# Kernel tuning notes

Measured on AMD Instinct MI355X. Metric: run time of the kernel, lower is better.

Reference implementation:

```python
import jax, jax.numpy as jnp
import numpy as np

KP_EXTENT = 0.05
N_Q = 40000   # query points
N_S = 40000   # support points
K = 32        # neighbors per query
P = 15        # kernel points
IN_DIM = 64
OUT_DIM = 128


def setup_inputs() -> dict:
    key = jax.random.key(0)
    k1, k2, k3, k4, k5, k6 = jax.random.split(key, 6)
    q_pts = jax.random.uniform(k1, (N_Q, 3), dtype=jnp.float32)
    s_pts = jax.random.uniform(k2, (N_S, 3), dtype=jnp.float32)
    # indices in [0, N_S]; value N_S hits the appended shadow row
    neighbor_idxs = jax.random.randint(k3, (N_Q, K), 0, N_S + 1)
    x = jax.random.normal(k4, (N_S, IN_DIM), dtype=jnp.float32)
    weights = jax.random.normal(k5, (P, IN_DIM, OUT_DIM), dtype=jnp.float32) * 0.05
    kernel_points = jax.random.normal(k6, (P, 3), dtype=jnp.float32) * 0.06
    return {"q_pts": q_pts, "s_pts": s_pts, "neighbor_idxs": neighbor_idxs,
            "x": x, "weights": weights, "kernel_points": kernel_points}


def reference(q_pts, s_pts, neighbor_idxs, x, weights, kernel_points):
    # Append shadow support point. NOTE: the original does
    # zeros_like(s_pts[:1,:] + 1e6) which is exactly zeros, so shadow = origin.
    s_pad = jnp.concatenate([s_pts, jnp.zeros_like(s_pts[:1, :])], axis=0)
    # Gather neighbor coordinates, center on queries: [N, K, 3]
    neighbors = s_pad[neighbor_idxs] - q_pts[:, None, :]
    # Distances to every kernel point: [N, K, P]
    diff = neighbors[:, :, None, :] - kernel_points[None, None, :, :]
    sq_distances = jnp.sum(diff * diff, axis=3)
    all_weights = jnp.clip(1.0 - jnp.sqrt(sq_distances) / KP_EXTENT, 0.0)
    all_weights = jnp.transpose(all_weights, (0, 2, 1))  # [N, P, K]
    # Gather neighbor features with zero shadow row: [N, K, D_in]
    feats = jnp.concatenate([x, jnp.zeros_like(x[:1, :])], axis=0)
    neighbors_x = feats[neighbor_idxs]
    # Kernel-point weighted aggregation: [N, P, D_in] -> [P, N, D_in]
    weighted_features = jnp.transpose(jnp.matmul(all_weights, neighbors_x), (1, 0, 2))
    # Per-kernel-point linear map: [P, N, D_out], then sum over kernel points
    kernel_outputs = jnp.matmul(weighted_features, weights)
    output_features = jnp.sum(kernel_outputs, axis=0)  # [N, D_out]
    # Normalize by count of "valid" neighbors (feature-sum > 0 heuristic)
    neighbor_features_sum = jnp.sum(neighbors_x, axis=-1)          # [N, K]
    neighbor_num = jnp.sum(neighbor_features_sum > 0.0, axis=-1)   # [N]
    neighbor_num = jnp.maximum(neighbor_num, 1).astype(output_features.dtype)
    return output_features / neighbor_num[:, None]
```

## Files before the change

kernel.cpp:

```cpp
#include <hip/hip_runtime.h>
#include <hip/hip_bf16.h>

#define N_Q     40000
#define N_S     40000
#define KK      32
#define PP      15
#define IN_DIM  64
#define OUT_DIM 128


__global__ __launch_bounds__(256) void prep_kernel(
    const float* __restrict__ x, const float* __restrict__ s_pts,
    const float* __restrict__ weights,
    float4* __restrict__ packed, __hip_bfloat162* __restrict__ wbf) {
  const int b = blockIdx.x;
  if (b < 2500) {
    const int t = b * 256 + threadIdx.x;
    const int row = t >> 4;
    const int sub = t & 15;
    float4 v = reinterpret_cast<const float4*>(x + (size_t)row * IN_DIM)[sub];
    float s = (v.x + v.y) + (v.z + v.w);
    s += __shfl_xor(s, 1, 64);
    s += __shfl_xor(s, 2, 64);
    s += __shfl_xor(s, 4, 64);
    s += __shfl_xor(s, 8, 64);
    if (sub == 0) {
      float4 pkt;
      pkt.x = s_pts[row * 3 + 0];
      pkt.y = s_pts[row * 3 + 1];
      pkt.z = s_pts[row * 3 + 2];
      pkt.w = (s > 0.0f) ? 1.0f : 0.0f;
      packed[row] = pkt;
    }
    if (t == 1) {
      float4 z; z.x = 0.f; z.y = 0.f; z.z = 0.f; z.w = 0.f;
      packed[N_S] = z;
    }
  } else {
    const int t = (b - 2500) * 256 + threadIdx.x;
    float2 w2 = reinterpret_cast<const float2*>(weights)[t];
    __hip_bfloat162 h;
    h.x = __float2bfloat16(w2.x);
    h.y = __float2bfloat16(w2.y);
    wbf[t] = h;
  }
}

__global__ __launch_bounds__(256) void kpconv_fused_kernel(
    const float* __restrict__ q_pts, const int* __restrict__ nidx,
    const float* __restrict__ x, const float* __restrict__ kpts,
    const float4* __restrict__ packed, const __hip_bfloat162* __restrict__ wbf,
    float* __restrict__ out) {
  const int tid  = blockIdx.x * 256 + threadIdx.x;
  const int lane = threadIdx.x & 63;
  const int n  = tid >> 5;
  const int nA = (tid & ~63) >> 5;

  float kx[PP], ky[PP], kz[PP];
  #pragma unroll
  for (int p = 0; p < PP; ++p) {
    kx[p] = kpts[p * 3 + 0];
    ky[p] = kpts[p * 3 + 1];
    kz[p] = kpts[p * 3 + 2];
  }

  const int id = nidx[tid];
  const float4 sp = packed[id];
  const bool real = (id < N_S);

  const float ox = sp.x - q_pts[n * 3 + 0];
  const float oy = sp.y - q_pts[n * 3 + 1];
  const float oz = sp.z - q_pts[n * 3 + 2];

  unsigned long long bal = __ballot(sp.w != 0.0f);
  unsigned int half = (lane < 32) ? (unsigned int)bal
                                  : (unsigned int)(bal >> 32);
  int num = (int)__popc(half);
  if (num < 1) num = 1;
  const float invnum = 1.0f / (float)num;

  float a0 = 0.f, a1 = 0.f;
  float b0 = 0.f, b1 = 0.f;

  #pragma unroll
  for (int p = 0; p < PP; ++p) {
    const float dx = ox - kx[p];
    const float dy = oy - ky[p];
    const float dz = oz - kz[p];
    const float d2 = dx * dx + dy * dy + dz * dz;
    const bool hit = real && (d2 < 0.0025f);
    unsigned long long b2 = __ballot(hit);
    if (b2 != 0ull) {
      const float wn = hit ? (1.0f - 20.0f * sqrtf(d2)) * invnum : 0.0f;
      while (b2) {
        const int j = __ffsll(b2) - 1;
        b2 &= b2 - 1;
        const float wj  = __shfl(wn, j);
        const int   idj = __shfl(id, j);
        const float* xr = x + (size_t)idj * IN_DIM;
        const __hip_bfloat162* wp =
            wbf + (size_t)p * (IN_DIM * OUT_DIM / 2) + lane;
        float h0 = 0.f, h1 = 0.f;
        #pragma unroll 4
        for (int d4 = 0; d4 < IN_DIM / 4; ++d4) {
          const float4 xv4 =
              *reinterpret_cast<const float4*>(xr + 4 * d4);
          #pragma unroll
          for (int dd = 0; dd < 4; ++dd) {
            const int d = 4 * d4 + dd;
            const __hip_bfloat162 w2 = wp[(size_t)d * (OUT_DIM / 2)];
            const float xd = (dd == 0) ? xv4.x : (dd == 1) ? xv4.y
                           : (dd == 2) ? xv4.z : xv4.w;
            h0 += xd * __bfloat162float(w2.x);
            h1 += xd * __bfloat162float(w2.y);
          }
        }
        if (j < 32) { a0 += wj * h0; a1 += wj * h1; }
        else        { b0 += wj * h0; b1 += wj * h1; }
      }
    }
  }

  float2 ra; ra.x = a0; ra.y = a1;
  float2 rb; rb.x = b0; rb.y = b1;
  *reinterpret_cast<float2*>(out + (size_t)nA * OUT_DIM + 2 * lane) = ra;
  *reinterpret_cast<float2*>(out + (size_t)(nA + 1) * OUT_DIM + 2 * lane) = rb;
}

extern "C" void kernel_launch(void* const* d_in, const int* in_sizes, int n_in,
                              void* d_out, int out_size, void* d_ws, size_t ws_size,
                              hipStream_t stream) {
  const float* q_pts   = (const float*)d_in[0];
  const float* s_pts   = (const float*)d_in[1];
  const int*   nidx    = (const int*)d_in[2];
  const float* x       = (const float*)d_in[3];
  const float* weights = (const float*)d_in[4];
  const float* kpts    = (const float*)d_in[5];
  float* out = (float*)d_out;

  char* ws = (char*)d_ws;
  float4*          packed = (float4*)ws;
  __hip_bfloat162* wbf    = (__hip_bfloat162*)(ws + (1u << 20));

  prep_kernel<<<2740, 256, 0, stream>>>(x, s_pts, weights, packed, wbf);
  kpconv_fused_kernel<<<(N_Q * KK) / 256, 256, 0, stream>>>(
      q_pts, nidx, x, kpts, packed, wbf, out);
}
```

Measured before the change: 105.1 us.

## Use bf16 MFMA for per-hit feature projection and prefilter neighbors by radius

```diff
diff --git a/kernel.cpp b/kernel.cpp
--- a/kernel.cpp
+++ b/kernel.cpp
@@ -1,5 +1,4 @@
 #include <hip/hip_runtime.h>
-#include <hip/hip_bf16.h>
 
 #define N_Q     40000
 #define N_S     40000
@@ -8,11 +7,20 @@
 #define IN_DIM  64
 #define OUT_DIM 128
 
+typedef __attribute__((ext_vector_type(8))) short short8;
+typedef __attribute__((ext_vector_type(4))) float floatx4;
+
+static __device__ __forceinline__ short f2bf(float f) {
+  union { float f; unsigned u; } v; v.f = f;
+  unsigned r = v.u + 0x7FFFu + ((v.u >> 16) & 1u);
+  return (short)(r >> 16);
+}
+
 
 __global__ __launch_bounds__(256) void prep_kernel(
     const float* __restrict__ x, const float* __restrict__ s_pts,
     const float* __restrict__ weights,
-    float4* __restrict__ packed, __hip_bfloat162* __restrict__ wbf) {
+    float4* __restrict__ packed, unsigned* __restrict__ wmf) {
   const int b = blockIdx.x;
   if (b < 2500) {
     const int t = b * 256 + threadIdx.x;
@@ -38,31 +46,39 @@
     }
   } else {
     const int t = (b - 2500) * 256 + threadIdx.x;
-    float2 w2 = reinterpret_cast<const float2*>(weights)[t];
-    __hip_bfloat162 h;
-    h.x = __float2bfloat16(w2.x);
-    h.y = __float2bfloat16(w2.y);
-    wbf[t] = h;
+    const int j2   = t & 3;
+    const int lane = (t >> 2) & 63;
+    const int fi   = t >> 8;
+    const int kc = fi & 1, g = (fi >> 1) & 7, p = fi >> 4;
+    const int c  = g * 16 + (lane & 15);
+    const int k0 = kc * 32 + (lane >> 4) * 8 + 2 * j2;
+    const float w0 = weights[(size_t)p * (IN_DIM * OUT_DIM) + (size_t)k0 * OUT_DIM + c];
+    const float w1 = weights[(size_t)p * (IN_DIM * OUT_DIM) + (size_t)(k0 + 1) * OUT_DIM + c];
+    wmf[t] = (unsigned)(unsigned short)f2bf(w0)
+           | ((unsigned)(unsigned short)f2bf(w1) << 16);
   }
 }
 
-__global__ __launch_bounds__(256) void kpconv_fused_kernel(
+__global__ __launch_bounds__(256, 4) void kpconv_fused_kernel(
     const float* __restrict__ q_pts, const int* __restrict__ nidx,
     const float* __restrict__ x, const float* __restrict__ kpts,
-    const float4* __restrict__ packed, const __hip_bfloat162* __restrict__ wbf,
+    const float4* __restrict__ packed, const uint4* __restrict__ wmf4,
     float* __restrict__ out) {
   const int tid  = blockIdx.x * 256 + threadIdx.x;
   const int lane = threadIdx.x & 63;
   const int n  = tid >> 5;
   const int nA = (tid & ~63) >> 5;
 
-  float kx[PP], ky[PP], kz[PP];
+  const int pl = (lane < PP) ? lane : 0;
+  const float kxl = kpts[pl * 3 + 0];
+  const float kyl = kpts[pl * 3 + 1];
+  const float kzl = kpts[pl * 3 + 2];
+
+  float r2 = kxl * kxl + kyl * kyl + kzl * kzl;
   #pragma unroll
-  for (int p = 0; p < PP; ++p) {
-    kx[p] = kpts[p * 3 + 0];
-    ky[p] = kpts[p * 3 + 1];
-    kz[p] = kpts[p * 3 + 2];
-  }
+  for (int s = 32; s; s >>= 1) r2 = fmaxf(r2, __shfl_xor(r2, s, 64));
+  const float R  = sqrtf(r2) + 0.05f;
+  const float R2 = R * R;
 
   const int id = nidx[tid];
   const float4 sp = packed[id];
@@ -79,52 +95,66 @@
   if (num < 1) num = 1;
   const float invnum = 1.0f / (float)num;
 
-  float a0 = 0.f, a1 = 0.f;
-  float b0 = 0.f, b1 = 0.f;
+  floatx4 acc[8];
+  #pragma unroll
+  for (int g = 0; g < 8; ++g) acc[g] = (floatx4){0.f, 0.f, 0.f, 0.f};
 
-  #pragma unroll
-  for (int p = 0; p < PP; ++p) {
-    const float dx = ox - kx[p];
-    const float dy = oy - ky[p];
-    const float dz = oz - kz[p];
+  const float d2o = ox * ox + oy * oy + oz * oz;
+  unsigned long long bc = __ballot(real && (d2o <= R2));
+  while (bc) {
+    const int j = (int)__ffsll((unsigned long long)bc) - 1;
+    bc &= bc - 1;
+    const float oxj = __shfl(ox, j);
+    const float oyj = __shfl(oy, j);
+    const float ozj = __shfl(oz, j);
+    const int   idj = __shfl(id, j);
+    const float inj = __shfl(invnum, j);
+    const float dx = oxj - kxl, dy = oyj - kyl, dz = ozj - kzl;
     const float d2 = dx * dx + dy * dy + dz * dz;
-    const bool hit = real && (d2 < 0.0025f);
-    unsigned long long b2 = __ballot(hit);
-    if (b2 != 0ull) {
-      const float wn = hit ? (1.0f - 20.0f * sqrtf(d2)) * invnum : 0.0f;
-      while (b2) {
-        const int j = __ffsll(b2) - 1;
-        b2 &= b2 - 1;
-        const float wj  = __shfl(wn, j);
-        const int   idj = __shfl(id, j);
-        const float* xr = x + (size_t)idj * IN_DIM;
-        const __hip_bfloat162* wp =
-            wbf + (size_t)p * (IN_DIM * OUT_DIM / 2) + lane;
-        float h0 = 0.f, h1 = 0.f;
-        #pragma unroll 4
-        for (int d4 = 0; d4 < IN_DIM / 4; ++d4) {
-          const float4 xv4 =
-              *reinterpret_cast<const float4*>(xr + 4 * d4);
-          #pragma unroll
-          for (int dd = 0; dd < 4; ++dd) {
-            const int d = 4 * d4 + dd;
-            const __hip_bfloat162 w2 = wp[(size_t)d * (OUT_DIM / 2)];
-            const float xd = (dd == 0) ? xv4.x : (dd == 1) ? xv4.y
-                           : (dd == 2) ? xv4.z : xv4.w;
-            h0 += xd * __bfloat162float(w2.x);
-            h1 += xd * __bfloat162float(w2.y);
-          }
-        }
-        if (j < 32) { a0 += wj * h0; a1 += wj * h1; }
-        else        { b0 += wj * h0; b1 += wj * h1; }
+    const bool hit = (lane < PP) && (d2 < 0.0025f);
+    const float wc = hit ? (1.0f - 20.0f * sqrtf(d2)) * inj : 0.0f;
+    unsigned long long bh = __ballot(hit);
+    const int m = j >> 5;
+    while (bh) {
+      const int h = (int)__ffsll((unsigned long long)bh) - 1;
+      bh &= bh - 1;
+      const float wj = __shfl(wc, h);
+      const int p = h;
+      short8 af0 = {0, 0, 0, 0, 0, 0, 0, 0};
+      short8 af1 = {0, 0, 0, 0, 0, 0, 0, 0};
+      if ((lane & 15) == m) {
+        const float4* xr = reinterpret_cast<const float4*>(x + (size_t)idj * IN_DIM);
+        const int q4 = (lane >> 4) * 2;
+        const float4 xa = xr[q4],     xb = xr[q4 + 1];
+        const float4 xc = xr[q4 + 8], xd = xr[q4 + 9];
+        af0[0] = f2bf(wj * xa.x); af0[1] = f2bf(wj * xa.y);
+        af0[2] = f2bf(wj * xa.z); af0[3] = f2bf(wj * xa.w);
+        af0[4] = f2bf(wj * xb.x); af0[5] = f2bf(wj * xb.y);
+        af0[6] = f2bf(wj * xb.z); af0[7] = f2bf(wj * xb.w);
+        af1[0] = f2bf(wj * xc.x); af1[1] = f2bf(wj * xc.y);
+        af1[2] = f2bf(wj * xc.z); af1[3] = f2bf(wj * xc.w);
+        af1[4] = f2bf(wj * xd.x); af1[5] = f2bf(wj * xd.y);
+        af1[6] = f2bf(wj * xd.z); af1[7] = f2bf(wj * xd.w);
+      }
+      #pragma unroll
+      for (int g = 0; g < 8; ++g) {
+        const uint4 b0 = wmf4[(size_t)((p * 8 + g) * 2 + 0) * 64 + lane];
+        acc[g] = __builtin_amdgcn_mfma_f32_16x16x32_bf16(
+            af0, __builtin_bit_cast(short8, b0), acc[g], 0, 0, 0);
+        const uint4 b1 = wmf4[(size_t)((p * 8 + g) * 2 + 1) * 64 + lane];
+        acc[g] = __builtin_amdgcn_mfma_f32_16x16x32_bf16(
+            af1, __builtin_bit_cast(short8, b1), acc[g], 0, 0, 0);
       }
     }
   }
 
-  float2 ra; ra.x = a0; ra.y = a1;
-  float2 rb; rb.x = b0; rb.y = b1;
-  *reinterpret_cast<float2*>(out + (size_t)nA * OUT_DIM + 2 * lane) = ra;
-  *reinterpret_cast<float2*>(out + (size_t)(nA + 1) * OUT_DIM + 2 * lane) = rb;
+  if (lane < 16) {
+    #pragma unroll
+    for (int g = 0; g < 8; ++g) {
+      out[(size_t)nA * OUT_DIM + g * 16 + lane]       = acc[g][0];
+      out[(size_t)(nA + 1) * OUT_DIM + g * 16 + lane] = acc[g][1];
+    }
+  }
 }
 
 extern "C" void kernel_launch(void* const* d_in, const int* in_sizes, int n_in,
@@ -139,10 +169,10 @@
   float* out = (float*)d_out;
 
   char* ws = (char*)d_ws;
-  float4*          packed = (float4*)ws;
-  __hip_bfloat162* wbf    = (__hip_bfloat162*)(ws + (1u << 20));
+  float4*   packed = (float4*)ws;
+  unsigned* wmf    = (unsigned*)(ws + (1u << 20));
 
-  prep_kernel<<<2740, 256, 0, stream>>>(x, s_pts, weights, packed, wbf);
+  prep_kernel<<<2740, 256, 0, stream>>>(x, s_pts, weights, packed, wmf);
   kpconv_fused_kernel<<<(N_Q * KK) / 256, 256, 0, stream>>>(
-      q_pts, nidx, x, kpts, packed, wbf, out);
+      q_pts, nidx, x, kpts, packed, (const uint4*)wmf, out);
 }
```

Result: faster. 99.78 us (-5.0%).
